# Kernel optimization log

Hardware: AMD Instinct MI355X
Metric: run time of the kernel (lower is better)

The kernel has to match this reference:

```python
import jax, jax.numpy as jnp
import numpy as np

N, IN_DIM, IN_F, OUT_DIM, OUT_F = 16, 32, 192, 32, 192
NUM_LAYERS = 4  # min_num_layers = max_num_layers = 4 (deterministic)
EPS = 1e-5


def setup_inputs() -> dict:
    key = jax.random.key(0)
    ks = jax.random.split(key, 9)
    mk = lambda k, s: jax.random.normal(k, s, dtype=jnp.float32)
    return {
        "x": mk(ks[0], (N, IN_DIM, IN_F)),
        # source_to_target parameter: (in_dim, in_features, out_features, out_dim)
        "s2t": mk(ks[1], (IN_DIM, IN_F, OUT_F, OUT_DIM)),
        # target_to_source parameter: (out_dim, out_features, in_features, in_dim)
        "t2s": mk(ks[2], (OUT_DIM, OUT_F, IN_F, IN_DIM)),
        # source_attention_mats: shapes alternate (out_f,in_f),(in_f,in_f),(out_f,in_f)
        "s0": mk(ks[3], (OUT_F, IN_F)),
        "s1": mk(ks[4], (IN_F, IN_F)),
        "s2": mk(ks[5], (OUT_F, IN_F)),
        # target_attention_mats: shapes alternate (in_f,out_f),(out_f,out_f),(in_f,out_f)
        "t0": mk(ks[6], (IN_F, OUT_F)),
        "t1": mk(ks[7], (OUT_F, OUT_F)),
        "t2": mk(ks[8], (IN_F, OUT_F)),
    }


def _layer_norm(y):
    # nn.LayerNorm over last two dims, elementwise_affine=False, eps=1e-5
    m = jnp.mean(y, axis=(-2, -1), keepdims=True)
    v = jnp.var(y, axis=(-2, -1), keepdims=True)
    return (y - m) / jnp.sqrt(v + EPS)


def _forward(x, s2t, t2s, src_mats, tgt_mats):
    history = [x]
    for i in range(1, NUM_LAYERS):
        ys = []
        for j in range(i):
            if i % 2 == 0 and j % 2 == 0:
                # source -> source: plain matmul with (in_f, in_f) transition mat
                ys.append(history[j] @ src_mats[(i - j - 1) % len(src_mats)])
            elif i % 2 == 0 and j % 2 != 0:
                # target -> source: fused weighted contraction
                # (t2s * A[..., None]) contracted with h over (d=out_dim, o=out_f),
                # then transpose(1,2): einsum directly yields (N, in_dim=e, in_f=f)
                A = src_mats[(i - j - 1) % len(src_mats)]  # (out_f, in_f)
                ys.append(jnp.einsum('ndo,dofe,of->nef', history[j], t2s, A))
            elif i % 2 != 0 and j % 2 == 0:
                # source -> target: fused weighted contraction -> (N, out_dim=d, out_f=o)
                A = tgt_mats[(i - j - 1) % len(tgt_mats)]  # (in_f, out_f)
                ys.append(jnp.einsum('nif,ifod,fo->ndo', history[j], s2t, A))
            else:
                # target -> target: plain matmul with (out_f, out_f) transition mat
                ys.append(history[j] @ tgt_mats[(i - j - 1) % len(tgt_mats)])
        y = sum(ys) / len(ys)  # torch.stack(...).mean(dim=0)
        y = _layer_norm(y)
        history.append(y)
    # return_layers='last-target'
    return history[-1]


def reference(x, s2t, t2s, s0, s1, s2, t0, t1, t2):
    return _forward(x, s2t, t2s, [s0, s1, s2], [t0, t1, t2])
```

## Files before the change

### kernel.cpp

```cpp
#include <hip/hip_runtime.h>

constexpr int NS   = 16;
constexpr int DIM  = 32;
constexpr int FEA  = 192;
constexpr int ELEMS = DIM * FEA;

constexpr int SPLIT   = 4;
constexpr int FPB     = FEA / SPLIT;
constexpr int FCHUNK  = 16;
constexpr int NCHUNKS = FPB / FCHUNK;
constexpr int ROWPAD  = 20;
constexpr int TPB     = 256;
constexpr int FSTRIDE = FEA * DIM;
constexpr int PREF    = 8;
constexpr int REDPAD  = 68;
constexpr int SITER   = (FCHUNK * DIM * NS / 4) / TPB;

typedef float vfloat4 __attribute__((ext_vector_type(4)));

__device__ __forceinline__ float4 ntload4(const float* p) {
    vfloat4 v = __builtin_nontemporal_load((const vfloat4*)p);
    return make_float4(v.x, v.y, v.z, v.w);
}

__device__ __forceinline__ void fma4(float4& a, float x, const float4& t) {
    a.x = fmaf(x, t.x, a.x);
    a.y = fmaf(x, t.y, a.y);
    a.z = fmaf(x, t.z, a.z);
    a.w = fmaf(x, t.w, a.w);
}

template <bool DUAL, bool LAST>
__device__ __forceinline__ void chunk_compute(
    const float* __restrict__ smem, const float* __restrict__ ac0,
    const float* __restrict__ ac1, int i,
    const float*& wp, float4 (&t)[PREF],
    float4* __restrict__ accA, float4* __restrict__ accB)
{
#pragma unroll
    for (int fl = 0; fl < FCHUNK; ++fl) {
        float4 cur = t[fl & (PREF - 1)];
        if (!LAST || fl < FCHUNK - PREF) {
            t[fl & (PREF - 1)] = ntload4(wp);
            wp += FSTRIDE;
        }
        const float a1 = ac0[fl];
        float4 ta = make_float4(cur.x * a1, cur.y * a1, cur.z * a1, cur.w * a1);
        float4 tb;
        if (DUAL) {
            const float a2 = ac1[fl];
            tb = make_float4(cur.x * a2, cur.y * a2, cur.z * a2, cur.w * a2);
        }
        const float* xr = smem + (fl * DIM + i) * ROWPAD;
#pragma unroll
        for (int g = 0; g < 4; ++g) {
            float4 xv = *(const float4*)(xr + g * 4);
            fma4(accA[g * 4 + 0], xv.x, ta);
            fma4(accA[g * 4 + 1], xv.y, ta);
            fma4(accA[g * 4 + 2], xv.z, ta);
            fma4(accA[g * 4 + 3], xv.w, ta);
            if (DUAL) {
                fma4(accB[g * 4 + 0], xv.x, tb);
                fma4(accB[g * 4 + 1], xv.y, tb);
                fma4(accB[g * 4 + 2], xv.z, tb);
                fma4(accB[g * 4 + 3], xv.w, tb);
            }
        }
    }
}

template <bool DUAL>
__global__ __launch_bounds__(TPB) void epass_kernel(
    const float* __restrict__ W, const float* __restrict__ X,
    const float* __restrict__ A1, const float* __restrict__ A2,
    float* __restrict__ outA, float* __restrict__ outB)
{
    __shared__ float smem[FCHUNK * DIM * ROWPAD];
    __shared__ float acol[2][FPB];

    const int tid = threadIdx.x;
    const int o   = blockIdx.x >> 2;
    const int s   = blockIdx.x & (SPLIT - 1);
    const int dq  = tid & 7;
    const int i   = tid >> 3;
    const int fBase = s * FPB;

    if (tid < FPB) {
        acol[0][tid] = A1[(fBase + tid) * FEA + o];
        if (DUAL) acol[1][tid] = A2[(fBase + tid) * FEA + o];
    }

    float4 accA[16];
    float4 accB[16];
#pragma unroll
    for (int n = 0; n < 16; ++n) {
        accA[n] = make_float4(0.f, 0.f, 0.f, 0.f);
        if (DUAL) accB[n] = make_float4(0.f, 0.f, 0.f, 0.f);
    }

    const float* wp = W + (size_t)(((i * FEA + fBase) * FEA + o) * DIM + dq * 4);
    float4 t[PREF];
#pragma unroll
    for (int k = 0; k < PREF; ++k) {
        t[k] = ntload4(wp);
        wp += FSTRIDE;
    }

    for (int c = 0; c < NCHUNKS; ++c) {
        __syncthreads();
#pragma unroll
        for (int r = 0; r < SITER; ++r) {
            int q  = r * TPB + tid;
            int nn = q >> 7;
            int ii = (q >> 2) & 31;
            int fq = q & 3;
            float4 v = *(const float4*)(X + (size_t)(nn * DIM + ii) * FEA
                                          + fBase + c * FCHUNK + fq * 4);
            smem[((fq * 4 + 0) * DIM + ii) * ROWPAD + nn] = v.x;
            smem[((fq * 4 + 1) * DIM + ii) * ROWPAD + nn] = v.y;
            smem[((fq * 4 + 2) * DIM + ii) * ROWPAD + nn] = v.z;
            smem[((fq * 4 + 3) * DIM + ii) * ROWPAD + nn] = v.w;
        }
        __syncthreads();

        const float* ac0 = &acol[0][c * FCHUNK];
        const float* ac1 = &acol[1][c * FCHUNK];
        if (c < NCHUNKS - 1)
            chunk_compute<DUAL, false>(smem, ac0, ac1, i, wp, t, accA, accB);
        else
            chunk_compute<DUAL, true>(smem, ac0, ac1, i, wp, t, accA, accB);
    }

#pragma unroll
    for (int n = 0; n < 16; ++n) {
        accA[n].x += __shfl_xor(accA[n].x, 32);
        accA[n].y += __shfl_xor(accA[n].y, 32);
        accA[n].z += __shfl_xor(accA[n].z, 32);
        accA[n].w += __shfl_xor(accA[n].w, 32);
        if (DUAL) {
            accB[n].x += __shfl_xor(accB[n].x, 32);
            accB[n].y += __shfl_xor(accB[n].y, 32);
            accB[n].z += __shfl_xor(accB[n].z, 32);
            accB[n].w += __shfl_xor(accB[n].w, 32);
        }
    }

    const int lane = tid & 63;
    const int wv   = tid >> 6;
    const int row  = (wv * 4 + ((lane >> 3) & 3)) * 8 + (lane & 7);
    float* red = smem;

    __syncthreads();
    if (!(lane & 32)) {
#pragma unroll
        for (int n = 0; n < 16; ++n)
            *(float4*)&red[row * REDPAD + n * 4] = accA[n];
    }
    __syncthreads();
#pragma unroll
    for (int h = 0; h < 2; ++h) {
        const int e = h * TPB + tid;
        const int n = e >> 5, d = e & 31;
        float v = 0.f;
#pragma unroll
        for (int w2 = 0; w2 < 16; ++w2)
            v += red[(w2 * 8 + (d >> 2)) * REDPAD + n * 4 + (d & 3)];
        outA[(size_t)(s * FEA + o) * (NS * DIM) + e] = v;
    }
    if (DUAL) {
        __syncthreads();
        if (!(lane & 32)) {
#pragma unroll
            for (int n = 0; n < 16; ++n)
                *(float4*)&red[row * REDPAD + n * 4] = accB[n];
        }
        __syncthreads();
#pragma unroll
        for (int h = 0; h < 2; ++h) {
            const int e = h * TPB + tid;
            const int n = e >> 5, d = e & 31;
            float v = 0.f;
#pragma unroll
            for (int w2 = 0; w2 < 16; ++w2)
                v += red[(w2 * 8 + (d >> 2)) * REDPAD + n * 4 + (d & 3)];
            outB[(size_t)(s * FEA + o) * (NS * DIM) + e] = v;
        }
    }
}


__device__ __forceinline__ float2 ln_stats_512(float s1, float s2, int tid, float* red) {
#pragma unroll
    for (int m = 1; m < 64; m <<= 1) {
        s1 += __shfl_xor(s1, m);
        s2 += __shfl_xor(s2, m);
    }
    if ((tid & 63) == 0) {
        red[(tid >> 6) * 2]     = s1;
        red[(tid >> 6) * 2 + 1] = s2;
    }
    __syncthreads();
    float a = 0.f, b = 0.f;
#pragma unroll
    for (int ww = 0; ww < 8; ++ww) { a += red[ww * 2]; b += red[ww * 2 + 1]; }
    float mean = a * (1.0f / ELEMS);
    float var  = b * (1.0f / ELEMS) - mean * mean;
    return make_float2(mean, rsqrtf(var + 1e-5f));
}

__global__ __launch_bounds__(512) void reduce_ln_h1(
    const float* __restrict__ p, float* __restrict__ h1)
{
    __shared__ float vals[FEA * 33];
    __shared__ float red[16];
    const int n = blockIdx.x, tid = threadIdx.x;
    float s1 = 0.f, s2 = 0.f;
    for (int e = tid; e < ELEMS; e += 512) {
        int d = e & 31, o = e >> 5;
        float v = 0.f;
#pragma unroll
        for (int sp = 0; sp < SPLIT; ++sp)
            v += p[(size_t)(sp * FEA + o) * (NS * DIM) + n * DIM + d];
        vals[o * 33 + d] = v; s1 += v; s2 += v * v;
    }
    float2 mr = ln_stats_512(s1, s2, tid, red);
    for (int e = tid; e < ELEMS; e += 512) {
        int o = e % FEA, d = e / FEA;
        h1[(size_t)n * ELEMS + e] = (vals[o * 33 + d] - mr.x) * mr.y;
    }
}

__global__ __launch_bounds__(512) void reduce_ln_h2(
    const float* __restrict__ p, const float* __restrict__ xs1, float* __restrict__ h2)
{
    __shared__ float vals[FEA * 33];
    __shared__ float red[16];
    const int n = blockIdx.x, tid = threadIdx.x;
    for (int e = tid; e < ELEMS; e += 512) {
        int d = e & 31, o = e >> 5;
        float v = 0.f;
#pragma unroll
        for (int sp = 0; sp < SPLIT; ++sp)
            v += p[(size_t)(sp * FEA + o) * (NS * DIM) + n * DIM + d];
        vals[o * 33 + d] = v;
    }
    __syncthreads();
    float s1 = 0.f, s2 = 0.f;
    for (int e = tid; e < ELEMS; e += 512) {
        int o = e % FEA, d = e / FEA;
        float v = 0.5f * (vals[o * 33 + d] + xs1[(size_t)n * ELEMS + e]);
        vals[o * 33 + d] = v; s1 += v; s2 += v * v;
    }
    float2 mr = ln_stats_512(s1, s2, tid, red);
    for (int e = tid; e < ELEMS; e += 512) {
        int o = e % FEA, d = e / FEA;
        h2[(size_t)n * ELEMS + e] = (vals[o * 33 + d] - mr.x) * mr.y;
    }
}

__global__ __launch_bounds__(512) void final_ln(
    const float* __restrict__ pB, const float* __restrict__ pD,
    const float* __restrict__ h1t1, float* __restrict__ out)
{
    __shared__ float vals[FEA * 33];
    __shared__ float red[16];
    const int n = blockIdx.x, tid = threadIdx.x;
    for (int e = tid; e < ELEMS; e += 512) {
        int d = e & 31, o = e >> 5;
        float v = 0.f;
#pragma unroll
        for (int sp = 0; sp < SPLIT; ++sp) {
            v += pB[(size_t)(sp * FEA + o) * (NS * DIM) + n * DIM + d];
            v += pD[(size_t)(sp * FEA + o) * (NS * DIM) + n * DIM + d];
        }
        vals[o * 33 + d] = v;
    }
    __syncthreads();
    float s1 = 0.f, s2 = 0.f;
    for (int e = tid; e < ELEMS; e += 512) {
        int o = e % FEA, d = e / FEA;
        float v = (vals[o * 33 + d] + h1t1[(size_t)n * ELEMS + e]) * (1.0f / 3.0f);
        vals[o * 33 + d] = v; s1 += v; s2 += v * v;
    }
    float2 mr = ln_stats_512(s1, s2, tid, red);
    for (int e = tid; e < ELEMS; e += 512) {
        int o = e % FEA, d = e / FEA;
        out[(size_t)n * ELEMS + e] = (vals[o * 33 + d] - mr.x) * mr.y;
    }
}

__global__ __launch_bounds__(192) void mm192x8(
    const float* __restrict__ X, const float* __restrict__ M, float* __restrict__ Y)
{
    __shared__ float rows[8][192];
    const int rb = blockIdx.x * 8;
    const int j  = threadIdx.x;
#pragma unroll
    for (int k = 0; k < 8; ++k) rows[k][j] = X[(rb + k) * 192 + j];
    __syncthreads();
    float acc[8] = {0.f, 0.f, 0.f, 0.f, 0.f, 0.f, 0.f, 0.f};
    for (int f = 0; f < 192; ++f) {
        float m = M[f * 192 + j];
#pragma unroll
        for (int k = 0; k < 8; ++k) acc[k] = fmaf(rows[k][f], m, acc[k]);
    }
#pragma unroll
    for (int k = 0; k < 8; ++k) Y[(rb + k) * 192 + j] = acc[k];
}

extern "C" void kernel_launch(void* const* d_in, const int* in_sizes, int n_in,
                              void* d_out, int out_size, void* d_ws, size_t ws_size,
                              hipStream_t stream) {
    (void)in_sizes; (void)n_in; (void)out_size; (void)ws_size;
    const float* x   = (const float*)d_in[0];
    const float* s2t = (const float*)d_in[1];
    const float* t2s = (const float*)d_in[2];
    const float* s0  = (const float*)d_in[3];
    const float* s1  = (const float*)d_in[4];
    const float* t0  = (const float*)d_in[6];
    const float* t1  = (const float*)d_in[7];
    const float* t2  = (const float*)d_in[8];
    float* out = (float*)d_out;

    float* ws = (float*)d_ws;
    float* xs1  = ws; ws += 98304;
    float* h1   = ws; ws += 98304;
    float* h1t1 = ws; ws += 98304;
    float* h2   = ws; ws += 98304;
    float* P    = ws; ws += SPLIT * FEA * NS * DIM;
    float* pB   = ws; ws += SPLIT * FEA * NS * DIM;

    mm192x8<<<64, 192, 0, stream>>>(x, s1, xs1);

    epass_kernel<true><<<SPLIT * FEA, TPB, 0, stream>>>(s2t, x, t0, t2, P, pB);
    reduce_ln_h1<<<16, 512, 0, stream>>>(P, h1);

    mm192x8<<<64, 192, 0, stream>>>(h1, t1, h1t1);

    epass_kernel<false><<<SPLIT * FEA, TPB, 0, stream>>>(t2s, h1, s0, nullptr, P, nullptr);
    reduce_ln_h2<<<16, 512, 0, stream>>>(P, xs1, h2);

    epass_kernel<false><<<SPLIT * FEA, TPB, 0, stream>>>(s2t, h2, t0, nullptr, P, nullptr);

    final_ln<<<16, 512, 0, stream>>>(pB, P, h1t1, out);
}
```

Baseline: 496.5 us.

## Retile weight-streaming contraction over o-ranges with 32-way i/f split

The einsum kernel now gives each block 8 output features, 4 input dims and 48 f values, so a wave reads 64 contiguous float4 of W per f step instead of 8 strided float4 per thread. X is staged once per block with no chunk loop, and cross-wave reduction goes through shared memory. Partial results grow from 4 to 32 splits, so the LayerNorm kernels now sum 32 partials per element using vectorized float4 loads. This is meant to improve coalescing of the large weight stream, at the cost of more partial-sum traffic and only 4 prefetched loads in flight per thread.

```diff
diff --git a/kernel.cpp b/kernel.cpp
--- a/kernel.cpp
+++ b/kernel.cpp
@@ -5,16 +5,13 @@
 constexpr int FEA  = 192;
 constexpr int ELEMS = DIM * FEA;
 
-constexpr int SPLIT   = 4;
-constexpr int FPB     = FEA / SPLIT;
-constexpr int FCHUNK  = 16;
-constexpr int NCHUNKS = FPB / FCHUNK;
-constexpr int ROWPAD  = 20;
+constexpr int ORANGE  = 8;
+constexpr int OSPL    = FEA / ORANGE;
+constexpr int FPB     = 48;
+constexpr int RS      = 32;
 constexpr int TPB     = 256;
 constexpr int FSTRIDE = FEA * DIM;
-constexpr int PREF    = 8;
-constexpr int REDPAD  = 68;
-constexpr int SITER   = (FCHUNK * DIM * NS / 4) / TPB;
+constexpr int PSTRIDE = NS * DIM;
 
 typedef float vfloat4 __attribute__((ext_vector_type(4)));
 
@@ -30,41 +27,73 @@
     a.w = fmaf(x, t.w, a.w);
 }
 
-template <bool DUAL, bool LAST>
-__device__ __forceinline__ void chunk_compute(
-    const float* __restrict__ smem, const float* __restrict__ ac0,
-    const float* __restrict__ ac1, int i,
-    const float*& wp, float4 (&t)[PREF],
-    float4* __restrict__ accA, float4* __restrict__ accB)
-{
-#pragma unroll
-    for (int fl = 0; fl < FCHUNK; ++fl) {
-        float4 cur = t[fl & (PREF - 1)];
-        if (!LAST || fl < FCHUNK - PREF) {
-            t[fl & (PREF - 1)] = ntload4(wp);
-            wp += FSTRIDE;
+template <bool DUAL, bool LOAD>
+__device__ __forceinline__ void step(
+    float4& slot, int fl, const float* __restrict__ xrow,
+    const float* __restrict__ ac, int ol,
+    const float*& wp, float4* __restrict__ accA, float4* __restrict__ accB)
+{
+    float4 cur = slot;
+    if (LOAD) { slot = ntload4(wp); wp += FSTRIDE; }
+    const float a1 = ac[fl * ORANGE + ol];
+    float4 ta = make_float4(cur.x * a1, cur.y * a1, cur.z * a1, cur.w * a1);
+    float4 tb;
+    if (DUAL) {
+        const float a2 = ac[FPB * ORANGE + fl * ORANGE + ol];
+        tb = make_float4(cur.x * a2, cur.y * a2, cur.z * a2, cur.w * a2);
+    }
+    const float* xr = xrow + fl * NS;
+#pragma unroll
+    for (int g = 0; g < 4; ++g) {
+        float4 xv = *(const float4*)(xr + g * 4);
+        fma4(accA[g * 4 + 0], xv.x, ta);
+        fma4(accA[g * 4 + 1], xv.y, ta);
+        fma4(accA[g * 4 + 2], xv.z, ta);
+        fma4(accA[g * 4 + 3], xv.w, ta);
+        if (DUAL) {
+            fma4(accB[g * 4 + 0], xv.x, tb);
+            fma4(accB[g * 4 + 1], xv.y, tb);
+            fma4(accB[g * 4 + 2], xv.z, tb);
+            fma4(accB[g * 4 + 3], xv.w, tb);
         }
-        const float a1 = ac0[fl];
-        float4 ta = make_float4(cur.x * a1, cur.y * a1, cur.z * a1, cur.w * a1);
-        float4 tb;
-        if (DUAL) {
-            const float a2 = ac1[fl];
-            tb = make_float4(cur.x * a2, cur.y * a2, cur.z * a2, cur.w * a2);
+    }
+}
+
+__device__ __forceinline__ void wave_reduce_store(
+    float4* __restrict__ acc, float* __restrict__ red, int wv, int lane,
+    float* __restrict__ out, int r, int oBase, int ol, int dq)
+{
+    __syncthreads();
+    if (wv >= 2) {
+        float* d = red + (wv - 2) * 4096;
+#pragma unroll
+        for (int n = 0; n < 16; ++n)
+            *(float4*)(d + (n * 64 + lane) * 4) = acc[n];
+    }
+    __syncthreads();
+    if (wv < 2) {
+        const float* sp = red + wv * 4096;
+#pragma unroll
+        for (int n = 0; n < 16; ++n) {
+            float4 v = *(const float4*)(sp + (n * 64 + lane) * 4);
+            acc[n].x += v.x; acc[n].y += v.y; acc[n].z += v.z; acc[n].w += v.w;
         }
-        const float* xr = smem + (fl * DIM + i) * ROWPAD;
-#pragma unroll
-        for (int g = 0; g < 4; ++g) {
-            float4 xv = *(const float4*)(xr + g * 4);
-            fma4(accA[g * 4 + 0], xv.x, ta);
-            fma4(accA[g * 4 + 1], xv.y, ta);
-            fma4(accA[g * 4 + 2], xv.z, ta);
-            fma4(accA[g * 4 + 3], xv.w, ta);
-            if (DUAL) {
-                fma4(accB[g * 4 + 0], xv.x, tb);
-                fma4(accB[g * 4 + 1], xv.y, tb);
-                fma4(accB[g * 4 + 2], xv.z, tb);
-                fma4(accB[g * 4 + 3], xv.w, tb);
-            }
+    }
+    __syncthreads();
+    if (wv == 1) {
+#pragma unroll
+        for (int n = 0; n < 16; ++n)
+            *(float4*)(red + (n * 64 + lane) * 4) = acc[n];
+    }
+    __syncthreads();
+    if (wv == 0) {
+        float* po = out + (size_t)(r * FEA + oBase + ol) * PSTRIDE + dq * 4;
+#pragma unroll
+        for (int n = 0; n < 16; ++n) {
+            float4 v = *(const float4*)(red + (n * 64 + lane) * 4);
+            float4 w = make_float4(acc[n].x + v.x, acc[n].y + v.y,
+                                   acc[n].z + v.z, acc[n].w + v.w);
+            *(float4*)(po + n * DIM) = w;
         }
     }
 }
@@ -75,119 +104,82 @@
     const float* __restrict__ A1, const float* __restrict__ A2,
     float* __restrict__ outA, float* __restrict__ outB)
 {
-    __shared__ float smem[FCHUNK * DIM * ROWPAD];
-    __shared__ float acol[2][FPB];
-
-    const int tid = threadIdx.x;
-    const int o   = blockIdx.x >> 2;
-    const int s   = blockIdx.x & (SPLIT - 1);
-    const int dq  = tid & 7;
-    const int i   = tid >> 3;
-    const int fBase = s * FPB;
-
-    if (tid < FPB) {
-        acol[0][tid] = A1[(fBase + tid) * FEA + o];
-        if (DUAL) acol[1][tid] = A2[(fBase + tid) * FEA + o];
-    }
-
-    float4 accA[16];
-    float4 accB[16];
+    __shared__ float smem[8192];
+    float* xs = smem;
+    float* ac = smem + 3072;
+
+    const int tid  = threadIdx.x;
+    const int bid  = blockIdx.x;
+    const int r    = bid & 31;
+    const int oS   = bid >> 5;
+    const int iBase = (r >> 2) * 4;
+    const int fBase = (r & 3) * FPB;
+    const int oBase = oS * ORANGE;
+    const int wv   = tid >> 6;
+    const int lane = tid & 63;
+    const int ol   = lane >> 3;
+    const int dq   = lane & 7;
+    const int i    = iBase + wv;
+
+    const float* wp = W + ((size_t)(i * FEA + fBase) * FEA + oBase) * DIM + lane * 4;
+    float4 t0 = ntload4(wp); wp += FSTRIDE;
+    float4 t1 = ntload4(wp); wp += FSTRIDE;
+    float4 t2 = ntload4(wp); wp += FSTRIDE;
+    float4 t3 = ntload4(wp); wp += FSTRIDE;
+
+    for (int t = tid; t < FPB * ORANGE; t += TPB) {
+        int f = t >> 3, o = t & 7;
+        ac[t] = A1[(fBase + f) * FEA + oBase + o];
+        if (DUAL) ac[FPB * ORANGE + t] = A2[(fBase + f) * FEA + oBase + o];
+    }
+
+#pragma unroll
+    for (int it = 0; it < 3; ++it) {
+        int q  = it * TPB + tid;
+        int fq = q % 12;
+        int rem = q / 12;
+        int n  = rem & 15;
+        int il = rem >> 4;
+        float4 v = *(const float4*)(X + (size_t)(n * DIM + iBase + il) * FEA
+                                      + fBase + fq * 4);
+        float* dst = xs + (il * FPB + fq * 4) * NS + n;
+        dst[0]      = v.x;
+        dst[NS]     = v.y;
+        dst[2 * NS] = v.z;
+        dst[3 * NS] = v.w;
+    }
+
+    float4 accA[16], accB[16];
 #pragma unroll
     for (int n = 0; n < 16; ++n) {
         accA[n] = make_float4(0.f, 0.f, 0.f, 0.f);
         if (DUAL) accB[n] = make_float4(0.f, 0.f, 0.f, 0.f);
     }
 
-    const float* wp = W + (size_t)(((i * FEA + fBase) * FEA + o) * DIM + dq * 4);
-    float4 t[PREF];
-#pragma unroll
-    for (int k = 0; k < PREF; ++k) {
-        t[k] = ntload4(wp);
-        wp += FSTRIDE;
-    }
-
-    for (int c = 0; c < NCHUNKS; ++c) {
-        __syncthreads();
-#pragma unroll
-        for (int r = 0; r < SITER; ++r) {
-            int q  = r * TPB + tid;
-            int nn = q >> 7;
-            int ii = (q >> 2) & 31;
-            int fq = q & 3;
-            float4 v = *(const float4*)(X + (size_t)(nn * DIM + ii) * FEA
-                                          + fBase + c * FCHUNK + fq * 4);
-            smem[((fq * 4 + 0) * DIM + ii) * ROWPAD + nn] = v.x;
-            smem[((fq * 4 + 1) * DIM + ii) * ROWPAD + nn] = v.y;
-            smem[((fq * 4 + 2) * DIM + ii) * ROWPAD + nn] = v.z;
-            smem[((fq * 4 + 3) * DIM + ii) * ROWPAD + nn] = v.w;
-        }
-        __syncthreads();
-
-        const float* ac0 = &acol[0][c * FCHUNK];
-        const float* ac1 = &acol[1][c * FCHUNK];
-        if (c < NCHUNKS - 1)
-            chunk_compute<DUAL, false>(smem, ac0, ac1, i, wp, t, accA, accB);
-        else
-            chunk_compute<DUAL, true>(smem, ac0, ac1, i, wp, t, accA, accB);
-    }
-
-#pragma unroll
-    for (int n = 0; n < 16; ++n) {
-        accA[n].x += __shfl_xor(accA[n].x, 32);
-        accA[n].y += __shfl_xor(accA[n].y, 32);
-        accA[n].z += __shfl_xor(accA[n].z, 32);
-        accA[n].w += __shfl_xor(accA[n].w, 32);
-        if (DUAL) {
-            accB[n].x += __shfl_xor(accB[n].x, 32);
-            accB[n].y += __shfl_xor(accB[n].y, 32);
-            accB[n].z += __shfl_xor(accB[n].z, 32);
-            accB[n].w += __shfl_xor(accB[n].w, 32);
-        }
-    }
-
-    const int lane = tid & 63;
-    const int wv   = tid >> 6;
-    const int row  = (wv * 4 + ((lane >> 3) & 3)) * 8 + (lane & 7);
-    float* red = smem;
-
-    __syncthreads();
-    if (!(lane & 32)) {
-#pragma unroll
-        for (int n = 0; n < 16; ++n)
-            *(float4*)&red[row * REDPAD + n * 4] = accA[n];
-    }
-    __syncthreads();
-#pragma unroll
-    for (int h = 0; h < 2; ++h) {
-        const int e = h * TPB + tid;
-        const int n = e >> 5, d = e & 31;
-        float v = 0.f;
-#pragma unroll
-        for (int w2 = 0; w2 < 16; ++w2)
-            v += red[(w2 * 8 + (d >> 2)) * REDPAD + n * 4 + (d & 3)];
-        outA[(size_t)(s * FEA + o) * (NS * DIM) + e] = v;
-    }
-    if (DUAL) {
-        __syncthreads();
-        if (!(lane & 32)) {
-#pragma unroll
-            for (int n = 0; n < 16; ++n)
-                *(float4*)&red[row * REDPAD + n * 4] = accB[n];
-        }
-        __syncthreads();
-#pragma unroll
-        for (int h = 0; h < 2; ++h) {
-            const int e = h * TPB + tid;
-            const int n = e >> 5, d = e & 31;
-            float v = 0.f;
-#pragma unroll
-            for (int w2 = 0; w2 < 16; ++w2)
-                v += red[(w2 * 8 + (d >> 2)) * REDPAD + n * 4 + (d & 3)];
-            outB[(size_t)(s * FEA + o) * (NS * DIM) + e] = v;
-        }
-    }
-}
-
+    __syncthreads();
+
+    const float* xrow = xs + wv * (FPB * NS);
+    for (int f4 = 0; f4 < 11; ++f4) {
+        const int fl = f4 * 4;
+        step<DUAL, true>(t0, fl + 0, xrow, ac, ol, wp, accA, accB);
+        step<DUAL, true>(t1, fl + 1, xrow, ac, ol, wp, accA, accB);
+        step<DUAL, true>(t2, fl + 2, xrow, ac, ol, wp, accA, accB);
+        step<DUAL, true>(t3, fl + 3, xrow, ac, ol, wp, accA, accB);
+    }
+    step<DUAL, false>(t0, 44, xrow, ac, ol, wp, accA, accB);
+    step<DUAL, false>(t1, 45, xrow, ac, ol, wp, accA, accB);
+    step<DUAL, false>(t2, 46, xrow, ac, ol, wp, accA, accB);
+    step<DUAL, false>(t3, 47, xrow, ac, ol, wp, accA, accB);
+
+    wave_reduce_store(accA, smem, wv, lane, outA, r, oBase, ol, dq);
+    if (DUAL)
+        wave_reduce_store(accB, smem, wv, lane, outB, r, oBase, ol, dq);
+}
+
+
+__device__ __forceinline__ void acc4(float4& a, const float4 b) {
+    a.x += b.x; a.y += b.y; a.z += b.z; a.w += b.w;
+}
 
 __device__ __forceinline__ float2 ln_stats_512(float s1, float s2, int tid, float* red) {
 #pragma unroll
@@ -208,6 +200,15 @@
     return make_float2(mean, rsqrtf(var + 1e-5f));
 }
 
+__device__ __forceinline__ float4 sumP(const float* __restrict__ p, int n, int o, int d) {
+    const float* pp = p + (size_t)o * PSTRIDE + n * DIM + d;
+    float4 a = make_float4(0.f, 0.f, 0.f, 0.f);
+#pragma unroll
+    for (int sp = 0; sp < RS; ++sp)
+        acc4(a, *(const float4*)(pp + (size_t)sp * FEA * PSTRIDE));
+    return a;
+}
+
 __global__ __launch_bounds__(512) void reduce_ln_h1(
     const float* __restrict__ p, float* __restrict__ h1)
 {
@@ -215,13 +216,15 @@
     __shared__ float red[16];
     const int n = blockIdx.x, tid = threadIdx.x;
     float s1 = 0.f, s2 = 0.f;
-    for (int e = tid; e < ELEMS; e += 512) {
-        int d = e & 31, o = e >> 5;
-        float v = 0.f;
-#pragma unroll
-        for (int sp = 0; sp < SPLIT; ++sp)
-            v += p[(size_t)(sp * FEA + o) * (NS * DIM) + n * DIM + d];
-        vals[o * 33 + d] = v; s1 += v; s2 += v * v;
+    for (int b = tid * 4; b < ELEMS; b += 2048) {
+        int d = b & 31, o = b >> 5;
+        float4 a = sumP(p, n, o, d);
+        vals[o * 33 + d]     = a.x;
+        vals[o * 33 + d + 1] = a.y;
+        vals[o * 33 + d + 2] = a.z;
+        vals[o * 33 + d + 3] = a.w;
+        s1 += a.x + a.y + a.z + a.w;
+        s2 += a.x * a.x + a.y * a.y + a.z * a.z + a.w * a.w;
     }
     float2 mr = ln_stats_512(s1, s2, tid, red);
     for (int e = tid; e < ELEMS; e += 512) {
@@ -236,13 +239,13 @@
     __shared__ float vals[FEA * 33];
     __shared__ float red[16];
     const int n = blockIdx.x, tid = threadIdx.x;
-    for (int e = tid; e < ELEMS; e += 512) {
-        int d = e & 31, o = e >> 5;
-        float v = 0.f;
-#pragma unroll
-        for (int sp = 0; sp < SPLIT; ++sp)
-            v += p[(size_t)(sp * FEA + o) * (NS * DIM) + n * DIM + d];
-        vals[o * 33 + d] = v;
+    for (int b = tid * 4; b < ELEMS; b += 2048) {
+        int d = b & 31, o = b >> 5;
+        float4 a = sumP(p, n, o, d);
+        vals[o * 33 + d]     = a.x;
+        vals[o * 33 + d + 1] = a.y;
+        vals[o * 33 + d + 2] = a.z;
+        vals[o * 33 + d + 3] = a.w;
     }
     __syncthreads();
     float s1 = 0.f, s2 = 0.f;
@@ -265,15 +268,15 @@
     __shared__ float vals[FEA * 33];
     __shared__ float red[16];
     const int n = blockIdx.x, tid = threadIdx.x;
-    for (int e = tid; e < ELEMS; e += 512) {
-        int d = e & 31, o = e >> 5;
-        float v = 0.f;
-#pragma unroll
-        for (int sp = 0; sp < SPLIT; ++sp) {
-            v += pB[(size_t)(sp * FEA + o) * (NS * DIM) + n * DIM + d];
-            v += pD[(size_t)(sp * FEA + o) * (NS * DIM) + n * DIM + d];
-        }
-        vals[o * 33 + d] = v;
+    for (int b = tid * 4; b < ELEMS; b += 2048) {
+        int d = b & 31, o = b >> 5;
+        float4 a = sumP(pB, n, o, d);
+        float4 c = sumP(pD, n, o, d);
+        acc4(a, c);
+        vals[o * 33 + d]     = a.x;
+        vals[o * 33 + d + 1] = a.y;
+        vals[o * 33 + d + 2] = a.z;
+        vals[o * 33 + d + 3] = a.w;
     }
     __syncthreads();
     float s1 = 0.f, s2 = 0.f;
@@ -327,20 +330,20 @@
     float* h1   = ws; ws += 98304;
     float* h1t1 = ws; ws += 98304;
     float* h2   = ws; ws += 98304;
-    float* P    = ws; ws += SPLIT * FEA * NS * DIM;
-    float* pB   = ws; ws += SPLIT * FEA * NS * DIM;
+    float* P    = ws; ws += RS * FEA * NS * DIM;
+    float* pB   = ws; ws += RS * FEA * NS * DIM;
 
     mm192x8<<<64, 192, 0, stream>>>(x, s1, xs1);
 
-    epass_kernel<true><<<SPLIT * FEA, TPB, 0, stream>>>(s2t, x, t0, t2, P, pB);
+    epass_kernel<true><<<OSPL * RS, TPB, 0, stream>>>(s2t, x, t0, t2, P, pB);
     reduce_ln_h1<<<16, 512, 0, stream>>>(P, h1);
 
     mm192x8<<<64, 192, 0, stream>>>(h1, t1, h1t1);
 
-    epass_kernel<false><<<SPLIT * FEA, TPB, 0, stream>>>(t2s, h1, s0, nullptr, P, nullptr);
+    epass_kernel<false><<<OSPL * RS, TPB, 0, stream>>>(t2s, h1, s0, nullptr, P, nullptr);
     reduce_ln_h2<<<16, 512, 0, stream>>>(P, xs1, h2);
 
-    epass_kernel<false><<<SPLIT * FEA, TPB, 0, stream>>>(s2t, h2, t0, nullptr, P, nullptr);
+    epass_kernel<false><<<OSPL * RS, TPB, 0, stream>>>(s2t, h2, t0, nullptr, P, nullptr);
 
     final_ln<<<16, 512, 0, stream>>>(pB, P, h1t1, out);
 }
```

After: 472.3 us. 4.9% less time.
